# Kernel tuning notes

Measured on AMD Instinct MI355X. Metric: run time of the kernel, lower is better.

## Reference

```python
import jax, jax.numpy as jnp
import numpy as np

NEG = -1e9  # additive mask value


def _longformer_attn(x, kv_mask, Wq, bq, Wk, bk, Wv, bv, Wqg, bqg, Wkg, bkg, Wvg, bvg, Wo, bo, H, w, G):
    # x: [B, S, E]; kv_mask: [B, S] (mask*-1 > 0 => global; first G tokens are global by construction)
    B, S, E = x.shape
    D = E // H
    scale = 1.0 / float(D) ** 0.5

    def proj(W, b):  # -> [B, H, S, D]
        return (x @ W + b).reshape(B, S, H, D).transpose(0, 2, 1, 3)

    q = proj(Wq, bq) * scale
    k = proj(Wk, bk)
    v = proj(Wv, bv)

    nc = S // w  # number of query chunks of size w
    # banded keys/values: each chunk of w queries sees a 3w key band (prev/cur/next chunk)
    idx = (jnp.arange(nc) * w)[:, None] + jnp.arange(3 * w)[None, :]  # [nc, 3w] into padded seq

    def band(t):  # [B,H,S,D] -> [B,H,nc,3w,D]
        tp = jnp.pad(t, ((0, 0), (0, 0), (w, w), (0, 0)))
        return tp[:, :, idx, :]

    k3, v3 = band(k), band(v)
    qc = q.reshape(B, H, nc, w, D)
    s_win = jnp.einsum('bhcwd,bhced->bhcwe', qc, k3)  # [B,H,nc,w,3w]

    i = jnp.arange(w)[:, None]
    j = jnp.arange(3 * w)[None, :]
    rel_ok = (j >= i) & (j <= i + 2 * w)  # |key_pos - query_pos| <= w
    keypos = (jnp.arange(nc) * w)[:, None, None] + (jnp.arange(3 * w) - w)[None, None, :]  # [nc,1,3w]
    ok = rel_ok[None] & (keypos >= 0) & (keypos < S) & (keypos >= G)  # global keys handled separately
    s_win = jnp.where(ok[None, None], s_win, NEG)

    # every query also attends to the G global keys (standard projections)
    s_g = jnp.einsum('bhqd,bhgd->bhqg', q, k[:, :, :G])  # [B,H,S,G]
    s_all = jnp.concatenate([s_g, s_win.reshape(B, H, S, 3 * w)], axis=-1)
    p = jax.nn.softmax(s_all, axis=-1)  # joint softmax over global + window keys
    p_g, p_w = p[..., :G], p[..., G:].reshape(B, H, nc, w, 3 * w)

    out = jnp.einsum('bhcwe,bhced->bhcwd', p_w, v3).reshape(B, H, S, D)
    out = out + jnp.einsum('bhqg,bhgd->bhqd', p_g, v[:, :, :G])

    # global query rows: full attention over all tokens with the *global* projections
    qg = (x @ Wqg + bqg).reshape(B, S, H, D).transpose(0, 2, 1, 3)[:, :, :G] * scale
    kg = (x @ Wkg + bkg).reshape(B, S, H, D).transpose(0, 2, 1, 3)
    vg = (x @ Wvg + bvg).reshape(B, S, H, D).transpose(0, 2, 1, 3)
    pg = jax.nn.softmax(jnp.einsum('bhgd,bhsd->bhgs', qg, kg), axis=-1)  # [B,H,G,S]
    out = out.at[:, :, :G].set(jnp.einsum('bhgs,bhsd->bhgd', pg, vg))

    ctx = out.transpose(0, 2, 1, 3).reshape(B, S, E)
    return ctx @ Wo + bo  # wrapper's self.output Linear


def setup_inputs() -> dict:
    key = jax.random.key(0)
    B, S, E, H, w, G = 2, 4096, 1024, 16, 256, 64
    ks = jax.random.split(key, 20)
    x = jax.random.normal(ks[0], (B, S, E), dtype=jnp.float32)
    # key_value_states acts as the mask source: (kv * -1) > 0 marks global tokens
    kv = jnp.zeros((B, S), dtype=jnp.float32).at[:, :G].set(-1.0)

    def lin(k1, k2):
        return (jax.random.normal(k1, (E, E), dtype=jnp.float32) * 0.02,
                jax.random.normal(k2, (E,), dtype=jnp.float32) * 0.02)

    Wq, bq = lin(ks[1], ks[2])
    Wk, bk = lin(ks[3], ks[4])
    Wv, bv = lin(ks[5], ks[6])
    Wqg, bqg = lin(ks[7], ks[8])
    Wkg, bkg = lin(ks[9], ks[10])
    Wvg, bvg = lin(ks[11], ks[12])
    Wo, bo = lin(ks[13], ks[14])
    return {"hidden_states": x, "key_value_states": kv,
            "Wq": Wq, "bq": bq, "Wk": Wk, "bk": bk, "Wv": Wv, "bv": bv,
            "Wqg": Wqg, "bqg": bqg, "Wkg": Wkg, "bkg": bkg, "Wvg": Wvg, "bvg": bvg,
            "Wo": Wo, "bo": bo, "num_heads": H, "window": w, "num_global": G}


def reference(hidden_states, key_value_states, Wq, bq, Wk, bk, Wv, bv, Wqg, bqg, Wkg, bkg, Wvg, bvg, Wo, bo, num_heads, window, num_global):
    return _longformer_attn(hidden_states, key_value_states, Wq, bq, Wk, bk, Wv, bv,
                            Wqg, bqg, Wkg, bkg, Wvg, bvg, Wo, bo,
                            num_heads, window, num_global)
```

## Files before the change

### kernel.cpp

```cpp
#include <hip/hip_runtime.h>

typedef _Float16 half_t;
typedef _Float16 h8 __attribute__((ext_vector_type(8)));
typedef _Float16 h4 __attribute__((ext_vector_type(4)));
typedef float f4 __attribute__((ext_vector_type(4)));

#define DEV __device__ __forceinline__

constexpr int Bc = 2, Sc = 4096, Ec = 1024, Hc = 16, Dc = 64, Wc = 256, Gc = 64;
constexpr float QSCALE = 0.125f;
constexpr float NEGV = -1e9f;

DEV f4 mfma16(h8 a, h8 b, f4 c) {
  return __builtin_amdgcn_mfma_f32_16x16x32_f16(a, b, c, 0, 0, 0);
}

DEV void gl_lds16(const half_t* g, half_t* l) {
  __builtin_amdgcn_global_load_lds((const __attribute__((address_space(1))) void*)g,
                                   (__attribute__((address_space(3))) void*)l, 16, 0, 0);
}

#define BARx() asm volatile("s_barrier" ::: "memory")
#define VMW(N) asm volatile("s_waitcnt vmcnt(" #N ")" ::: "memory")

__global__ void prep(const float* __restrict__ x,
                     const float* __restrict__ Wq, const float* __restrict__ Wk,
                     const float* __restrict__ Wv, const float* __restrict__ Wkg,
                     const float* __restrict__ Wvg, const float* __restrict__ Wqg,
                     const float* __restrict__ Wo,
                     half_t* __restrict__ xh, half_t* __restrict__ Wcat,
                     half_t* __restrict__ WtO) {
  __shared__ float tile[64][65];
  const int bx = blockIdx.x;
  if (bx < 8192) {
    int i = bx * 256 + threadIdx.x;
    float4 v = ((const float4*)x)[i];
    h4 o;
    o[0] = (half_t)v.x; o[1] = (half_t)v.y; o[2] = (half_t)v.z; o[3] = (half_t)v.w;
    ((h4*)xh)[i] = o;
    return;
  }
  const int widx = bx - 8192;
  const int y = widx >> 8;
  const int xb = widx & 255;
  const float* W = (y == 0) ? Wq : (y == 1) ? Wk : (y == 2) ? Wv :
                   (y == 3) ? Wkg : (y == 4) ? Wvg : (y == 5) ? Wqg : Wo;
  half_t* Wt = (y < 6) ? (Wcat + (size_t)y * Ec * Ec) : WtO;
  const int bxt = xb & 15, byt = xb >> 4;
  const int tx = threadIdx.x & 63, ty = threadIdx.x >> 6;
  const int n0 = bxt * 64, k0 = byt * 64;
#pragma unroll
  for (int i = 0; i < 16; ++i) {
    int k = ty + i * 4;
    tile[k][tx] = W[(size_t)(k0 + k) * Ec + n0 + tx];
  }
  __syncthreads();
#pragma unroll
  for (int i = 0; i < 16; ++i) {
    int n = ty + i * 4;
    Wt[(size_t)(n0 + n) * Ec + k0 + tx] = (half_t)tile[tx][n];
  }
}

__global__ __launch_bounds__(256) void gemm_proj(const half_t* __restrict__ A,
                                                 const half_t* __restrict__ Bt,
                                                 const float* __restrict__ bq,
                                                 const float* __restrict__ bk,
                                                 const float* __restrict__ bv,
                                                 const float* __restrict__ bkg,
                                                 const float* __restrict__ bvg,
                                                 const float* __restrict__ bqg,
                                                 half_t* __restrict__ qh, half_t* __restrict__ kh,
                                                 half_t* __restrict__ vt, half_t* __restrict__ kgh,
                                                 half_t* __restrict__ vgt, half_t* __restrict__ qgh) {
  __shared__ __align__(16) half_t Ash[3][4096];
  __shared__ __align__(16) half_t Bsh[3][4096];
  const bool qgblk = (blockIdx.y == 64);
  if (qgblk && blockIdx.x >= 8) return;
  const int tid = threadIdx.x;
  const int wv = tid >> 6, lane = tid & 63;
  const int mr = lane & 15, qd = lane >> 4;
  const int wv_m = wv >> 1, wv_n = wv & 1;
  const int col0 = qgblk ? (5 * Ec + (int)blockIdx.x * 128) : (int)blockIdx.x * 128;
  const int row0 = qgblk ? 0 : (int)blockIdx.y * 128;
  const int g = col0 >> 10;

  const half_t* sA[2];
  const half_t* sB[2];
  int dsto[2];
#pragma unroll
  for (int i = 0; i < 2; ++i) {
    const int slot = wv * 128 + i * 64 + lane;
    const int r = slot >> 2;
    const int kc = (slot & 3) ^ ((r >> 1) & 3);
    const int ar = qgblk ? ((r < 64) ? r : 4032 + r) : (row0 + r);
    sA[i] = A + (size_t)ar * Ec + kc * 8;
    sB[i] = Bt + (size_t)(col0 + r) * Ec + kc * 8;
    dsto[i] = (wv * 128 + i * 64) * 8;
  }
  int aoff[4], boff[4];
#pragma unroll
  for (int mt = 0; mt < 4; ++mt) {
    const int r = wv_m * 64 + mt * 16 + mr;
    aoff[mt] = ((r << 2) | (qd ^ ((r >> 1) & 3))) * 8;
  }
#pragma unroll
  for (int nt = 0; nt < 4; ++nt) {
    const int r = wv_n * 64 + nt * 16 + mr;
    boff[nt] = ((r << 2) | (qd ^ ((r >> 1) & 3))) * 8;
  }

  f4 acc[4][4] = {};
  half_t *Ac = &Ash[0][0], *An = &Ash[1][0], *Aw = &Ash[2][0];
  half_t *Bc = &Bsh[0][0], *Bn = &Bsh[1][0], *Bw = &Bsh[2][0];

  auto stage = [&](half_t* da, half_t* db, int k0) {
#pragma unroll
    for (int i = 0; i < 2; ++i) {
      gl_lds16(sA[i] + k0, da + dsto[i]);
      gl_lds16(sB[i] + k0, db + dsto[i]);
    }
  };
  auto compute = [&](const half_t* ba, const half_t* bb) {
    h8 af[4], bf[4];
#pragma unroll
    for (int mt = 0; mt < 4; ++mt) af[mt] = *(const h8*)(ba + aoff[mt]);
#pragma unroll
    for (int nt = 0; nt < 4; ++nt) bf[nt] = *(const h8*)(bb + boff[nt]);
    __builtin_amdgcn_s_setprio(1);
#pragma unroll
    for (int mt = 0; mt < 4; ++mt)
#pragma unroll
      for (int nt = 0; nt < 4; ++nt)
        acc[mt][nt] = mfma16(af[mt], bf[nt], acc[mt][nt]);
    __builtin_amdgcn_s_setprio(0);
  };

  stage(Ac, Bc, 0);
  stage(An, Bn, 32);
  VMW(4);
  BARx();

  for (int kt = 0; kt < 30; ++kt) {
    stage(Aw, Bw, kt * 32 + 64);
    compute(Ac, Bc);
    VMW(4);
    BARx();
    half_t* t;
    t = Ac; Ac = An; An = Aw; Aw = t;
    t = Bc; Bc = Bn; Bn = Bw; Bw = t;
  }
  compute(Ac, Bc);
  VMW(0);
  BARx();
  compute(An, Bn);

  const float* bptr = (g == 0) ? bq : (g == 1) ? bk : (g == 2) ? bv :
                      (g == 3) ? bkg : (g == 4) ? bvg : bqg;
#pragma unroll
  for (int mt = 0; mt < 4; ++mt) {
#pragma unroll
    for (int nt = 0; nt < 4; ++nt) {
      const int C = col0 + wv_n * 64 + nt * 16 + mr;
      const int c1 = C & 1023, hh = c1 >> 6, d = c1 & 63;
      const float bval = bptr[c1];
      const int Rbase = row0 + wv_m * 64 + mt * 16 + qd * 4;
      f4 a = acc[mt][nt];
      if (g == 2 || g == 4) {
        half_t* O = (g == 2) ? vt : vgt;
        int b = Rbase >> 12, s = Rbase & 4095;
        h4 pk;
#pragma unroll
        for (int r = 0; r < 4; ++r) pk[r] = (half_t)(a[r] + bval);
        *(h4*)(O + ((size_t)(b * Hc + hh) * Dc + d) * Sc + s) = pk;
      } else if (g == 5) {
#pragma unroll
        for (int r = 0; r < 4; ++r) {
          int rr = Rbase + r;
          int b = rr >> 6, s = rr & 63;
          qgh[((size_t)(b * Hc + hh) * Gc + s) * Dc + d] = (half_t)((a[r] + bval) * QSCALE);
        }
      } else {
        half_t* O = (g == 0) ? qh : (g == 1) ? kh : kgh;
        const float scale = (g == 0) ? QSCALE : 1.0f;
#pragma unroll
        for (int r = 0; r < 4; ++r) {
          int R = Rbase + r;
          int b = R >> 12, s = R & 4095;
          O[((size_t)(b * Hc + hh) * Sc + s) * Dc + d] = (half_t)((a[r] + bval) * scale);
        }
      }
    }
  }
}

__global__ __launch_bounds__(256) void gemm_out(const half_t* __restrict__ A,
                                                const half_t* __restrict__ Bt,
                                                const float* __restrict__ bias,
                                                float* __restrict__ O) {
  __shared__ __align__(16) half_t Ash[3][4096];
  __shared__ __align__(16) half_t Bsh[3][4096];
  const int tid = threadIdx.x;
  const int wv = tid >> 6, lane = tid & 63;
  const int mr = lane & 15, qd = lane >> 4;
  const int wv_m = wv >> 1, wv_n = wv & 1;
  const int col0 = blockIdx.x * 128;
  const int row0 = blockIdx.y * 128;

  const half_t* sA[2];
  const half_t* sB[2];
  int dsto[2];
#pragma unroll
  for (int i = 0; i < 2; ++i) {
    const int slot = wv * 128 + i * 64 + lane;
    const int r = slot >> 2;
    const int kc = (slot & 3) ^ ((r >> 1) & 3);
    sA[i] = A + (size_t)(row0 + r) * Ec + kc * 8;
    sB[i] = Bt + (size_t)(col0 + r) * Ec + kc * 8;
    dsto[i] = (wv * 128 + i * 64) * 8;
  }
  int aoff[4], boff[4];
#pragma unroll
  for (int mt = 0; mt < 4; ++mt) {
    const int r = wv_m * 64 + mt * 16 + mr;
    aoff[mt] = ((r << 2) | (qd ^ ((r >> 1) & 3))) * 8;
  }
#pragma unroll
  for (int nt = 0; nt < 4; ++nt) {
    const int r = wv_n * 64 + nt * 16 + mr;
    boff[nt] = ((r << 2) | (qd ^ ((r >> 1) & 3))) * 8;
  }

  f4 acc[4][4] = {};
  half_t *Ac = &Ash[0][0], *An = &Ash[1][0], *Aw = &Ash[2][0];
  half_t *Bc = &Bsh[0][0], *Bn = &Bsh[1][0], *Bw = &Bsh[2][0];

  auto stage = [&](half_t* da, half_t* db, int k0) {
#pragma unroll
    for (int i = 0; i < 2; ++i) {
      gl_lds16(sA[i] + k0, da + dsto[i]);
      gl_lds16(sB[i] + k0, db + dsto[i]);
    }
  };
  auto compute = [&](const half_t* ba, const half_t* bb) {
    h8 af[4], bf[4];
#pragma unroll
    for (int mt = 0; mt < 4; ++mt) af[mt] = *(const h8*)(ba + aoff[mt]);
#pragma unroll
    for (int nt = 0; nt < 4; ++nt) bf[nt] = *(const h8*)(bb + boff[nt]);
    __builtin_amdgcn_s_setprio(1);
#pragma unroll
    for (int mt = 0; mt < 4; ++mt)
#pragma unroll
      for (int nt = 0; nt < 4; ++nt)
        acc[mt][nt] = mfma16(af[mt], bf[nt], acc[mt][nt]);
    __builtin_amdgcn_s_setprio(0);
  };

  stage(Ac, Bc, 0);
  stage(An, Bn, 32);
  VMW(4);
  BARx();

  for (int kt = 0; kt < 30; ++kt) {
    stage(Aw, Bw, kt * 32 + 64);
    compute(Ac, Bc);
    VMW(4);
    BARx();
    half_t* t;
    t = Ac; Ac = An; An = Aw; Aw = t;
    t = Bc; Bc = Bn; Bn = Bw; Bw = t;
  }
  compute(Ac, Bc);
  VMW(0);
  BARx();
  compute(An, Bn);

#pragma unroll
  for (int mt = 0; mt < 4; ++mt) {
#pragma unroll
    for (int nt = 0; nt < 4; ++nt) {
      const int C = col0 + wv_n * 64 + nt * 16 + mr;
      const float bval = bias[C];
      const int Rbase = row0 + wv_m * 64 + mt * 16 + qd * 4;
      f4 a = acc[mt][nt];
#pragma unroll
      for (int r = 0; r < 4; ++r)
        O[(size_t)(Rbase + r) * Ec + C] = a[r] + bval;
    }
  }
}

__global__ __launch_bounds__(256) void win_attn(const half_t* __restrict__ qh,
                                                const half_t* __restrict__ kh,
                                                const half_t* __restrict__ vt,
                                                half_t* __restrict__ ctx) {
  constexpr int PST = 88;
  __shared__ __align__(16) half_t Kb[2][64 * 64];
  __shared__ __align__(16) half_t Vb[2][64 * 64];
  __shared__ __align__(16) half_t Pl[4][16 * PST];
  const int bid = blockIdx.x;
  const int qc = bid & 15, h = (bid >> 4) & 15, b = bid >> 8;
  const int qs = qc << 8;
  const int tid = threadIdx.x, wv = tid >> 6, lane = tid & 63;
  const int mr = lane & 15, qd = lane >> 4;
  const int qw = qs + wv * 64;
  const size_t bh = (size_t)(b * Hc + h);
  const half_t* qb = qh + bh * Sc * Dc;
  const half_t* kb = kh + bh * Sc * Dc;
  const half_t* vb = vt + bh * Dc * Sc;
  half_t* Pw = &Pl[wv][0];

  h8 qf[4][2];
#pragma unroll
  for (int qt = 0; qt < 4; ++qt) {
    const half_t* qrow = qb + (size_t)(qw + qt * 16 + mr) * Dc;
    qf[qt][0] = *(const h8*)(qrow + qd * 8);
    qf[qt][1] = *(const h8*)(qrow + 32 + qd * 8);
  }

  int tiles[14];
  int nT = 0;
  tiles[nT++] = 0;
  {
    int lo = qs - Wc; if (lo < Gc) lo = Gc;
    int hi = qs + 448; if (hi > Sc - 64) hi = Sc - 64;
    for (int kp0 = lo; kp0 <= hi; kp0 += 64) tiles[nT++] = kp0;
  }

  auto stage = [&](int kp0, int bi) {
#pragma unroll
    for (int i = 0; i < 2; ++i) {
      const int seg = wv * 2 + i;
      const int s = seg * 64 + lane;
      const int r = s >> 3;
      const int kc = (s & 7) ^ (r & 7);
      gl_lds16(kb + (size_t)(kp0 + r) * Dc + kc * 8, &Kb[bi][seg * 512]);
      gl_lds16(vb + (size_t)r * Sc + kp0 + kc * 8, &Vb[bi][seg * 512]);
    }
  };

  float m_run[4], l_run[4];
  f4 acc[4][4] = {};
#pragma unroll
  for (int qt = 0; qt < 4; ++qt) { m_run[qt] = -1e30f; l_run[qt] = 0.f; }

  stage(tiles[0], 0);

  for (int t = 0; t < nT; ++t) {
    __syncthreads();
    if (t + 1 < nT) stage(tiles[t + 1], (t + 1) & 1);
    const int kp0 = tiles[t];
    if (t > 0 && (kp0 > qw + 319 || kp0 + 63 < qw - Wc)) continue;

    const half_t* BK = Kb[t & 1];
    const half_t* BV = Vb[t & 1];
    h8 kf[4][2], vf[4][2];
#pragma unroll
    for (int mt = 0; mt < 4; ++mt) {
      const int row = mt * 16 + mr, r7 = row & 7;
      kf[mt][0] = *(const h8*)(BK + (size_t)(row * 8 + (qd ^ r7)) * 8);
      kf[mt][1] = *(const h8*)(BK + (size_t)(row * 8 + ((qd + 4) ^ r7)) * 8);
      vf[mt][0] = *(const h8*)(BV + (size_t)(row * 8 + (qd ^ r7)) * 8);
      vf[mt][1] = *(const h8*)(BV + (size_t)(row * 8 + ((qd + 4) ^ r7)) * 8);
    }
    const bool nomask = (t == 0) || (kp0 >= qw - 193 && kp0 <= qw + 193);

#pragma unroll
    for (int qt = 0; qt < 4; ++qt) {
      f4 sa[4];
#pragma unroll
      for (int mt = 0; mt < 4; ++mt) {
        f4 s = {};
        s = mfma16(kf[mt][0], qf[qt][0], s);
        s = mfma16(kf[mt][1], qf[qt][1], s);
        sa[mt] = s;
      }
      const int q = qw + qt * 16 + mr;
      if (!nomask) {
#pragma unroll
        for (int mt = 0; mt < 4; ++mt)
#pragma unroll
          for (int r = 0; r < 4; ++r) {
            const int kp = kp0 + mt * 16 + qd * 4 + r;
            if (kp < q - Wc || kp > q + Wc) sa[mt][r] = NEGV;
          }
      }
      float tm = -1e30f;
#pragma unroll
      for (int mt = 0; mt < 4; ++mt)
#pragma unroll
        for (int r = 0; r < 4; ++r) tm = fmaxf(tm, sa[mt][r]);
      tm = fmaxf(tm, __shfl_xor(tm, 16));
      tm = fmaxf(tm, __shfl_xor(tm, 32));
      const float mnew = fmaxf(m_run[qt], tm);
      const float alpha = __expf(m_run[qt] - mnew);
      m_run[qt] = mnew;
      float psum = 0.0f;
#pragma unroll
      for (int mt = 0; mt < 4; ++mt) {
        h4 pk;
#pragma unroll
        for (int r = 0; r < 4; ++r) {
          const float p = __expf(sa[mt][r] - mnew);
          psum += p;
          pk[r] = (half_t)p;
        }
        *(h4*)(Pw + mr * PST + mt * 16 + qd * 4) = pk;
      }
      psum += __shfl_xor(psum, 16);
      psum += __shfl_xor(psum, 32);
      l_run[qt] = l_run[qt] * alpha + psum;
#pragma unroll
      for (int mt = 0; mt < 4; ++mt)
#pragma unroll
        for (int r = 0; r < 4; ++r) acc[qt][mt][r] *= alpha;
      const h8 p0 = *(const h8*)(Pw + mr * PST + qd * 8);
      const h8 p1 = *(const h8*)(Pw + mr * PST + 32 + qd * 8);
#pragma unroll
      for (int mt = 0; mt < 4; ++mt) {
        acc[qt][mt] = mfma16(vf[mt][0], p0, acc[qt][mt]);
        acc[qt][mt] = mfma16(vf[mt][1], p1, acc[qt][mt]);
      }
    }
  }

#pragma unroll
  for (int qt = 0; qt < 4; ++qt) {
    const float inv = 1.0f / l_run[qt];
    const int q = qw + qt * 16 + mr;
    half_t* crow = ctx + ((size_t)(b * Sc) + q) * Ec + h * Dc;
#pragma unroll
    for (int mt = 0; mt < 4; ++mt) {
      h4 pk;
#pragma unroll
      for (int r = 0; r < 4; ++r) pk[r] = (half_t)(acc[qt][mt][r] * inv);
      *(h4*)(crow + mt * 16 + qd * 4) = pk;
    }
  }
}

__global__ __launch_bounds__(256) void gq_part(const half_t* __restrict__ qgh,
                                               const half_t* __restrict__ kgh,
                                               const half_t* __restrict__ vgt,
                                               float* __restrict__ pm,
                                               float* __restrict__ pl,
                                               float* __restrict__ pacc) {
  constexpr int PST = 88;
  __shared__ __align__(16) half_t Pl[4][16 * PST];
  const int ch = blockIdx.x & 7, h = (blockIdx.x >> 3) & 15, b = blockIdx.x >> 7;
  const int tid = threadIdx.x, wv = tid >> 6, lane = tid & 63;
  const int mr = lane & 15, qd = lane >> 4;
  const size_t bh = (size_t)(b * Hc + h);
  const half_t* qb = qgh + bh * Gc * Dc;
  const half_t* kb = kgh + bh * Sc * Dc;
  const half_t* vb = vgt + bh * Dc * Sc;
  half_t* Pw = &Pl[wv][0];

  const int qrow = wv * 16 + mr;
  const h8 qf0 = *(const h8*)(qb + (size_t)qrow * Dc + qd * 8);
  const h8 qf1 = *(const h8*)(qb + (size_t)qrow * Dc + 32 + qd * 8);

  float m_run = -1e30f, l_run = 0.f;
  f4 acc[4] = {};

  for (int t = 0; t < 8; ++t) {
    const int kp0 = ch * 512 + t * 64;
    f4 sa[4];
#pragma unroll
    for (int mt = 0; mt < 4; ++mt) {
      const int kp = kp0 + mt * 16 + mr;
      h8 kf0 = *(const h8*)(kb + (size_t)kp * Dc + qd * 8);
      h8 kf1 = *(const h8*)(kb + (size_t)kp * Dc + 32 + qd * 8);
      f4 s = {};
      s = mfma16(kf0, qf0, s);
      s = mfma16(kf1, qf1, s);
      sa[mt] = s;
    }
    float tm = -1e30f;
#pragma unroll
    for (int mt = 0; mt < 4; ++mt)
#pragma unroll
      for (int r = 0; r < 4; ++r) tm = fmaxf(tm, sa[mt][r]);
    tm = fmaxf(tm, __shfl_xor(tm, 16));
    tm = fmaxf(tm, __shfl_xor(tm, 32));
    const float mnew = fmaxf(m_run, tm);
    const float alpha = __expf(m_run - mnew);
    m_run = mnew;
    float psum = 0.0f;
#pragma unroll
    for (int mt = 0; mt < 4; ++mt) {
      h4 pk;
#pragma unroll
      for (int r = 0; r < 4; ++r) {
        const float p = __expf(sa[mt][r] - mnew);
        psum += p;
        pk[r] = (half_t)p;
      }
      *(h4*)(Pw + mr * PST + mt * 16 + qd * 4) = pk;
    }
    psum += __shfl_xor(psum, 16);
    psum += __shfl_xor(psum, 32);
    l_run = l_run * alpha + psum;
#pragma unroll
    for (int mt = 0; mt < 4; ++mt)
#pragma unroll
      for (int r = 0; r < 4; ++r) acc[mt][r] *= alpha;
    const h8 p0 = *(const h8*)(Pw + mr * PST + qd * 8);
    const h8 p1 = *(const h8*)(Pw + mr * PST + 32 + qd * 8);
#pragma unroll
    for (int mt = 0; mt < 4; ++mt) {
      const h8 vf0 = *(const h8*)(vb + (size_t)(mt * 16 + mr) * Sc + kp0 + qd * 8);
      const h8 vf1 = *(const h8*)(vb + (size_t)(mt * 16 + mr) * Sc + kp0 + 32 + qd * 8);
      acc[mt] = mfma16(vf0, p0, acc[mt]);
      acc[mt] = mfma16(vf1, p1, acc[mt]);
    }
  }

  const size_t pidx = (bh * 8 + ch) * Gc + qrow;
  if (qd == 0) { pm[pidx] = m_run; pl[pidx] = l_run; }
  float* pa = pacc + pidx * Dc;
#pragma unroll
  for (int mt = 0; mt < 4; ++mt)
#pragma unroll
    for (int r = 0; r < 4; ++r)
      pa[mt * 16 + qd * 4 + r] = acc[mt][r];
}

__global__ __launch_bounds__(256) void gq_combine(const float* __restrict__ pm,
                                                  const float* __restrict__ pl,
                                                  const float* __restrict__ pacc,
                                                  half_t* __restrict__ ctx) {
  const int h = blockIdx.x & 15, b = blockIdx.x >> 4;
  const size_t bh = (size_t)(b * Hc + h);
  const int q = threadIdx.x >> 2, dg = (threadIdx.x & 3) * 16;
  float m[8];
  float M = -1e30f;
#pragma unroll
  for (int c = 0; c < 8; ++c) {
    m[c] = pm[(bh * 8 + c) * Gc + q];
    M = fmaxf(M, m[c]);
  }
  float denom = 0.f, num[16] = {};
#pragma unroll
  for (int c = 0; c < 8; ++c) {
    const float w = __expf(m[c] - M);
    denom += w * pl[(bh * 8 + c) * Gc + q];
    const float* pa = pacc + ((bh * 8 + c) * Gc + q) * Dc + dg;
#pragma unroll
    for (int j = 0; j < 16; ++j) num[j] += w * pa[j];
  }
  const float inv = 1.0f / denom;
  half_t* crow = ctx + ((size_t)(b * Sc) + q) * Ec + h * Dc + dg;
#pragma unroll
  for (int j = 0; j < 16; ++j) crow[j] = (half_t)(num[j] * inv);
}


extern "C" void kernel_launch(void* const* d_in, const int* in_sizes, int n_in,
                              void* d_out, int out_size, void* d_ws, size_t ws_size,
                              hipStream_t stream) {
  const float* x   = (const float*)d_in[0];
  const float* Wq  = (const float*)d_in[2];
  const float* bq  = (const float*)d_in[3];
  const float* Wk  = (const float*)d_in[4];
  const float* bk  = (const float*)d_in[5];
  const float* Wv  = (const float*)d_in[6];
  const float* bv  = (const float*)d_in[7];
  const float* Wqg = (const float*)d_in[8];
  const float* bqg = (const float*)d_in[9];
  const float* Wkg = (const float*)d_in[10];
  const float* bkg = (const float*)d_in[11];
  const float* Wvg = (const float*)d_in[12];
  const float* bvg = (const float*)d_in[13];
  const float* Wo  = (const float*)d_in[14];
  const float* bo  = (const float*)d_in[15];
  float* out = (float*)d_out;

  char* ws = (char*)d_ws;
  size_t off = 0;
  auto alloc = [&](size_t bytes) {
    void* p = ws + off;
    off = (off + bytes + 255) & ~(size_t)255;
    return p;
  };
  const size_t BSE2 = (size_t)Bc * Sc * Ec * 2;
  const size_t W2 = (size_t)Ec * Ec * 2;
  half_t* xh   = (half_t*)alloc(BSE2);
  half_t* Wcat = (half_t*)alloc(W2 * 6);
  half_t* WtO  = (half_t*)alloc(W2);
  half_t* qh   = (half_t*)alloc(BSE2);
  half_t* kh   = (half_t*)alloc(BSE2);
  half_t* vt   = (half_t*)alloc(BSE2);
  half_t* kgh  = (half_t*)alloc(BSE2);
  half_t* vgt  = (half_t*)alloc(BSE2);
  half_t* qgh  = (half_t*)alloc((size_t)Bc * Hc * Gc * Dc * 2);
  half_t* ctx  = (half_t*)alloc(BSE2);
  float*  pm   = (float*)alloc((size_t)Bc * Hc * 8 * Gc * 4);
  float*  pl   = (float*)alloc((size_t)Bc * Hc * 8 * Gc * 4);
  float*  pacc = (float*)alloc((size_t)Bc * Hc * 8 * Gc * Dc * 4);
  (void)ws_size; (void)in_sizes; (void)n_in; (void)out_size;

  prep<<<8192 + 7 * 256, 256, 0, stream>>>(x, Wq, Wk, Wv, Wkg, Wvg, Wqg, Wo,
                                           xh, Wcat, WtO);

  gemm_proj<<<dim3(40, 65), 256, 0, stream>>>(xh, Wcat, bq, bk, bv, bkg, bvg, bqg,
                                              qh, kh, vt, kgh, vgt, qgh);

  win_attn<<<Bc * Hc * (Sc / 256), 256, 0, stream>>>(qh, kh, vt, ctx);

  gq_part<<<Bc * Hc * 8, 256, 0, stream>>>(qgh, kgh, vgt, pm, pl, pacc);
  gq_combine<<<Bc * Hc, 256, 0, stream>>>(pm, pl, pacc, ctx);

  gemm_out<<<dim3(8, 64), 256, 0, stream>>>(ctx, WtO, bo, out);
}
```

Baseline: 396.3 us.

## Enlarge projection GEMM tile to 256x128 and unroll triple-buffer rotation

The projection GEMM now computes a 256x128 output tile per block instead of 128x128, with each wave holding 8x4 MFMA accumulators. This halves the grid rows and reuses each B tile across twice as many rows, which cuts global and LDS traffic per flop. Both GEMMs replace the rotating buffer pointers with a loop unrolled by three that uses fixed buffer addresses, and they gain occupancy hints in their launch bounds. In exchange, the larger accumulator array and LDS footprint raise register pressure and may lower occupancy. The global-query block masks out the extra rows it now loads.

```diff
diff --git a/kernel.cpp b/kernel.cpp
--- a/kernel.cpp
+++ b/kernel.cpp
@@ -62,46 +62,55 @@
   }
 }
 
-__global__ __launch_bounds__(256) void gemm_proj(const half_t* __restrict__ A,
-                                                 const half_t* __restrict__ Bt,
-                                                 const float* __restrict__ bq,
-                                                 const float* __restrict__ bk,
-                                                 const float* __restrict__ bv,
-                                                 const float* __restrict__ bkg,
-                                                 const float* __restrict__ bvg,
-                                                 const float* __restrict__ bqg,
-                                                 half_t* __restrict__ qh, half_t* __restrict__ kh,
-                                                 half_t* __restrict__ vt, half_t* __restrict__ kgh,
-                                                 half_t* __restrict__ vgt, half_t* __restrict__ qgh) {
-  __shared__ __align__(16) half_t Ash[3][4096];
+__global__ __launch_bounds__(256, 2) void gemm_proj(const half_t* __restrict__ A,
+                                                    const half_t* __restrict__ Bt,
+                                                    const float* __restrict__ bq,
+                                                    const float* __restrict__ bk,
+                                                    const float* __restrict__ bv,
+                                                    const float* __restrict__ bkg,
+                                                    const float* __restrict__ bvg,
+                                                    const float* __restrict__ bqg,
+                                                    half_t* __restrict__ qh, half_t* __restrict__ kh,
+                                                    half_t* __restrict__ vt, half_t* __restrict__ kgh,
+                                                    half_t* __restrict__ vgt, half_t* __restrict__ qgh) {
+  __shared__ __align__(16) half_t Ash[3][8192];
   __shared__ __align__(16) half_t Bsh[3][4096];
-  const bool qgblk = (blockIdx.y == 64);
+  const bool qgblk = (blockIdx.y == 32);
   if (qgblk && blockIdx.x >= 8) return;
   const int tid = threadIdx.x;
   const int wv = tid >> 6, lane = tid & 63;
   const int mr = lane & 15, qd = lane >> 4;
   const int wv_m = wv >> 1, wv_n = wv & 1;
   const int col0 = qgblk ? (5 * Ec + (int)blockIdx.x * 128) : (int)blockIdx.x * 128;
-  const int row0 = qgblk ? 0 : (int)blockIdx.y * 128;
+  const int row0 = qgblk ? 0 : (int)blockIdx.y * 256;
   const int g = col0 >> 10;
 
-  const half_t* sA[2];
+  const half_t* sA[4];
   const half_t* sB[2];
-  int dsto[2];
-#pragma unroll
-  for (int i = 0; i < 2; ++i) {
-    const int slot = wv * 128 + i * 64 + lane;
+  int dstoA[4], dstoB[2];
+#pragma unroll
+  for (int j = 0; j < 4; ++j) {
+    const int slot = j * 256 + tid;
     const int r = slot >> 2;
     const int kc = (slot & 3) ^ ((r >> 1) & 3);
-    const int ar = qgblk ? ((r < 64) ? r : 4032 + r) : (row0 + r);
-    sA[i] = A + (size_t)ar * Ec + kc * 8;
-    sB[i] = Bt + (size_t)(col0 + r) * Ec + kc * 8;
-    dsto[i] = (wv * 128 + i * 64) * 8;
-  }
-  int aoff[4], boff[4];
-#pragma unroll
-  for (int mt = 0; mt < 4; ++mt) {
-    const int r = wv_m * 64 + mt * 16 + mr;
+    int ar;
+    if (qgblk) { const int rm = r & 127; ar = (rm < 64) ? rm : 4032 + rm; }
+    else ar = row0 + r;
+    sA[j] = A + (size_t)ar * Ec + kc * 8;
+    dstoA[j] = slot * 8;
+  }
+#pragma unroll
+  for (int j = 0; j < 2; ++j) {
+    const int slot = j * 256 + tid;
+    const int r = slot >> 2;
+    const int kc = (slot & 3) ^ ((r >> 1) & 3);
+    sB[j] = Bt + (size_t)(col0 + r) * Ec + kc * 8;
+    dstoB[j] = slot * 8;
+  }
+  int aoff[8], boff[4];
+#pragma unroll
+  for (int mt = 0; mt < 8; ++mt) {
+    const int r = wv_m * 128 + mt * 16 + mr;
     aoff[mt] = ((r << 2) | (qd ^ ((r >> 1) & 3))) * 8;
   }
 #pragma unroll
@@ -110,61 +119,62 @@
     boff[nt] = ((r << 2) | (qd ^ ((r >> 1) & 3))) * 8;
   }
 
-  f4 acc[4][4] = {};
-  half_t *Ac = &Ash[0][0], *An = &Ash[1][0], *Aw = &Ash[2][0];
-  half_t *Bc = &Bsh[0][0], *Bn = &Bsh[1][0], *Bw = &Bsh[2][0];
+  f4 acc[8][4] = {};
 
   auto stage = [&](half_t* da, half_t* db, int k0) {
 #pragma unroll
-    for (int i = 0; i < 2; ++i) {
-      gl_lds16(sA[i] + k0, da + dsto[i]);
-      gl_lds16(sB[i] + k0, db + dsto[i]);
-    }
+    for (int j = 0; j < 4; ++j) gl_lds16(sA[j] + k0, da + dstoA[j]);
+#pragma unroll
+    for (int j = 0; j < 2; ++j) gl_lds16(sB[j] + k0, db + dstoB[j]);
   };
   auto compute = [&](const half_t* ba, const half_t* bb) {
-    h8 af[4], bf[4];
-#pragma unroll
-    for (int mt = 0; mt < 4; ++mt) af[mt] = *(const h8*)(ba + aoff[mt]);
+    h8 af[8], bf[4];
+#pragma unroll
+    for (int mt = 0; mt < 8; ++mt) af[mt] = *(const h8*)(ba + aoff[mt]);
 #pragma unroll
     for (int nt = 0; nt < 4; ++nt) bf[nt] = *(const h8*)(bb + boff[nt]);
     __builtin_amdgcn_s_setprio(1);
 #pragma unroll
-    for (int mt = 0; mt < 4; ++mt)
+    for (int mt = 0; mt < 8; ++mt)
 #pragma unroll
       for (int nt = 0; nt < 4; ++nt)
         acc[mt][nt] = mfma16(af[mt], bf[nt], acc[mt][nt]);
     __builtin_amdgcn_s_setprio(0);
   };
 
-  stage(Ac, Bc, 0);
-  stage(An, Bn, 32);
-  VMW(4);
+  stage(&Ash[0][0], &Bsh[0][0], 0);
+  stage(&Ash[1][0], &Bsh[1][0], 32);
+  VMW(6);
   BARx();
 
-  for (int kt = 0; kt < 30; ++kt) {
-    stage(Aw, Bw, kt * 32 + 64);
-    compute(Ac, Bc);
-    VMW(4);
-    BARx();
-    half_t* t;
-    t = Ac; Ac = An; An = Aw; Aw = t;
-    t = Bc; Bc = Bn; Bn = Bw; Bw = t;
-  }
-  compute(Ac, Bc);
+#pragma unroll 1
+  for (int it = 0; it < 10; ++it) {
+    const int kk = it * 96;
+    stage(&Ash[2][0], &Bsh[2][0], kk + 64);
+    compute(&Ash[0][0], &Bsh[0][0]);
+    VMW(6); BARx();
+    stage(&Ash[0][0], &Bsh[0][0], kk + 96);
+    compute(&Ash[1][0], &Bsh[1][0]);
+    VMW(6); BARx();
+    stage(&Ash[1][0], &Bsh[1][0], kk + 128);
+    compute(&Ash[2][0], &Bsh[2][0]);
+    VMW(6); BARx();
+  }
+  compute(&Ash[0][0], &Bsh[0][0]);
   VMW(0);
   BARx();
-  compute(An, Bn);
+  compute(&Ash[1][0], &Bsh[1][0]);
 
   const float* bptr = (g == 0) ? bq : (g == 1) ? bk : (g == 2) ? bv :
                       (g == 3) ? bkg : (g == 4) ? bvg : bqg;
 #pragma unroll
-  for (int mt = 0; mt < 4; ++mt) {
+  for (int mt = 0; mt < 8; ++mt) {
 #pragma unroll
     for (int nt = 0; nt < 4; ++nt) {
       const int C = col0 + wv_n * 64 + nt * 16 + mr;
       const int c1 = C & 1023, hh = c1 >> 6, d = c1 & 63;
       const float bval = bptr[c1];
-      const int Rbase = row0 + wv_m * 64 + mt * 16 + qd * 4;
+      const int Rbase = row0 + wv_m * 128 + mt * 16 + qd * 4;
       f4 a = acc[mt][nt];
       if (g == 2 || g == 4) {
         half_t* O = (g == 2) ? vt : vgt;
@@ -177,8 +187,10 @@
 #pragma unroll
         for (int r = 0; r < 4; ++r) {
           int rr = Rbase + r;
-          int b = rr >> 6, s = rr & 63;
-          qgh[((size_t)(b * Hc + hh) * Gc + s) * Dc + d] = (half_t)((a[r] + bval) * QSCALE);
+          if (rr < 128) {
+            int b = rr >> 6, s = rr & 63;
+            qgh[((size_t)(b * Hc + hh) * Gc + s) * Dc + d] = (half_t)((a[r] + bval) * QSCALE);
+          }
         }
       } else {
         half_t* O = (g == 0) ? qh : (g == 1) ? kh : kgh;
@@ -194,10 +206,10 @@
   }
 }
 
-__global__ __launch_bounds__(256) void gemm_out(const half_t* __restrict__ A,
-                                                const half_t* __restrict__ Bt,
-                                                const float* __restrict__ bias,
-                                                float* __restrict__ O) {
+__global__ __launch_bounds__(256, 3) void gemm_out(const half_t* __restrict__ A,
+                                                   const half_t* __restrict__ Bt,
+                                                   const float* __restrict__ bias,
+                                                   float* __restrict__ O) {
   __shared__ __align__(16) half_t Ash[3][4096];
   __shared__ __align__(16) half_t Bsh[3][4096];
   const int tid = threadIdx.x;
@@ -232,8 +244,6 @@
   }
 
   f4 acc[4][4] = {};
-  half_t *Ac = &Ash[0][0], *An = &Ash[1][0], *Aw = &Ash[2][0];
-  half_t *Bc = &Bsh[0][0], *Bn = &Bsh[1][0], *Bw = &Bsh[2][0];
 
   auto stage = [&](half_t* da, half_t* db, int k0) {
 #pragma unroll
@@ -257,24 +267,28 @@
     __builtin_amdgcn_s_setprio(0);
   };
 
-  stage(Ac, Bc, 0);
-  stage(An, Bn, 32);
+  stage(&Ash[0][0], &Bsh[0][0], 0);
+  stage(&Ash[1][0], &Bsh[1][0], 32);
   VMW(4);
   BARx();
 
-  for (int kt = 0; kt < 30; ++kt) {
-    stage(Aw, Bw, kt * 32 + 64);
-    compute(Ac, Bc);
-    VMW(4);
-    BARx();
-    half_t* t;
-    t = Ac; Ac = An; An = Aw; Aw = t;
-    t = Bc; Bc = Bn; Bn = Bw; Bw = t;
-  }
-  compute(Ac, Bc);
+#pragma unroll 1
+  for (int it = 0; it < 10; ++it) {
+    const int kk = it * 96;
+    stage(&Ash[2][0], &Bsh[2][0], kk + 64);
+    compute(&Ash[0][0], &Bsh[0][0]);
+    VMW(4); BARx();
+    stage(&Ash[0][0], &Bsh[0][0], kk + 96);
+    compute(&Ash[1][0], &Bsh[1][0]);
+    VMW(4); BARx();
+    stage(&Ash[1][0], &Bsh[1][0], kk + 128);
+    compute(&Ash[2][0], &Bsh[2][0]);
+    VMW(4); BARx();
+  }
+  compute(&Ash[0][0], &Bsh[0][0]);
   VMW(0);
   BARx();
-  compute(An, Bn);
+  compute(&Ash[1][0], &Bsh[1][0]);
 
 #pragma unroll
   for (int mt = 0; mt < 4; ++mt) {
@@ -324,8 +338,8 @@
   tiles[nT++] = 0;
   {
     int lo = qs - Wc; if (lo < Gc) lo = Gc;
-    int hi = qs + 448; if (hi > Sc - 64) hi = Sc - 64;
-    for (int kp0 = lo; kp0 <= hi; kp0 += 64) tiles[nT++] = kp0;
+    int hi2 = qs + 448; if (hi2 > Sc - 64) hi2 = Sc - 64;
+    for (int kp0 = lo; kp0 <= hi2; kp0 += 64) tiles[nT++] = kp0;
   }
 
   auto stage = [&](int kp0, int bi) {
@@ -604,7 +618,7 @@
   prep<<<8192 + 7 * 256, 256, 0, stream>>>(x, Wq, Wk, Wv, Wkg, Wvg, Wqg, Wo,
                                            xh, Wcat, WtO);
 
-  gemm_proj<<<dim3(40, 65), 256, 0, stream>>>(xh, Wcat, bq, bk, bv, bkg, bvg, bqg,
+  gemm_proj<<<dim3(40, 33), 256, 0, stream>>>(xh, Wcat, bq, bk, bv, bkg, bvg, bqg,
                                               qh, kh, vt, kgh, vgt, qgh);
 
   win_attn<<<Bc * Hc * (Sc / 256), 256, 0, stream>>>(qh, kh, vt, ctx);
```

Measured after the change: 399.8 us. About the same (+0.9%).
